# Optimization experiments

Hardware: AMD Instinct MI355X
Metric: run time of the kernel (lower is better)

## Reference

```python
import jax, jax.numpy as jnp
import numpy as np
from math import sqrt, pi

EMBED, HEADS, ATTN, MLP = 1024, 16, 1024, 4096
HEAD_DIM = ATTN // HEADS
EPS = 1e-5

def _ln(x):
    mu = jnp.mean(x, axis=-1, keepdims=True)
    var = jnp.var(x, axis=-1, keepdims=True)
    return (x - mu) / jnp.sqrt(var + EPS)

def _gelu(x):
    return 0.5 * x * (1.0 + jnp.tanh(sqrt(2.0 / pi) * (x + 0.044715 * x**3)))

def setup_inputs() -> dict:
    key = jax.random.key(0)
    ks = jax.random.split(key, 6)
    B, S = 2, 2048
    x = jax.random.normal(ks[0], (B, S, EMBED), dtype=jnp.float32)
    # weights stored as [in, out] (transpose of torch's [out, in]); math identical
    w_qkv = jax.random.normal(ks[1], (EMBED, 3 * ATTN), dtype=jnp.float32) / sqrt(EMBED)
    w_fc = jax.random.normal(ks[2], (ATTN, EMBED), dtype=jnp.float32) / sqrt(ATTN)
    w1 = jax.random.normal(ks[3], (EMBED, MLP), dtype=jnp.float32) / sqrt(EMBED)
    b1 = jnp.zeros((MLP,), dtype=jnp.float32)
    w2 = jax.random.normal(ks[4], (MLP, EMBED), dtype=jnp.float32) / sqrt(MLP)
    b2 = jnp.zeros((EMBED,), dtype=jnp.float32)
    return {"x": x, "w_qkv": w_qkv, "w_fc": w_fc, "w1": w1, "b1": b1, "w2": w2, "b2": b2}

def reference(x, w_qkv, w_fc, w1, b1, w2, b2):
    B, S, _ = x.shape
    res = x
    h = _ln(x)
    qkv = h @ w_qkv                                   # [B,S,3*ATTN]
    q, k, v = jnp.split(qkv, 3, axis=-1)
    q = q.reshape(B, S, HEADS, HEAD_DIM)
    k = k.reshape(B, S, HEADS, HEAD_DIM)
    v = v.reshape(B, S, HEADS, HEAD_DIM)
    attn = jnp.einsum('bqnc,bknc->bnqk', q, k) / sqrt(HEAD_DIM)  # [B,H,S,S]
    attn = jax.nn.softmax(attn, axis=-1)
    attn_val = jnp.einsum('bnqk,bknc->bqnc', attn, v).reshape(B, S, ATTN)
    x = res + attn_val @ w_fc
    res = x
    h = _ln(x)
    h = _gelu(h @ w1 + b1) @ w2 + b2
    return res + h
```

## Files before the change

### kernel.cpp

```cpp
#include <hip/hip_runtime.h>

typedef unsigned short u16;
typedef __attribute__((ext_vector_type(8))) short bf16x8;
typedef __attribute__((ext_vector_type(4))) short s16x4;
typedef __attribute__((ext_vector_type(4))) float f32x4;

#define DEV __device__ __forceinline__

DEV u16 f2bf(float f) {
  union { float f; unsigned u; } v; v.f = f;
  unsigned r = v.u + 0x7fffu + ((v.u >> 16) & 1u);
  return (u16)(r >> 16);
}
DEV u16 f2bf_tr(float f) {
  union { float f; unsigned u; } v; v.f = f;
  return (u16)(v.u >> 16);
}

DEV int swzi(int row, int col) { return row * 64 + (col ^ ((row & 7) << 3)); }

DEV void gl16(const u16* g, u16* l) {
  __builtin_amdgcn_global_load_lds((const __attribute__((address_space(1))) void*)g,
                                   (__attribute__((address_space(3))) void*)l, 16, 0, 0);
}

template <int N> DEV void waitv() {
  asm volatile("s_waitcnt vmcnt(%0)" :: "n"(N) : "memory");
}

__global__ __launch_bounds__(256) void wcastT(const float* __restrict__ w,
                                              u16* __restrict__ wt, int K, int N) {
  __shared__ float t[32][33];
  int n0 = blockIdx.x * 32, k0 = blockIdx.y * 32;
  int tx = threadIdx.x & 31, ty = threadIdx.x >> 5;
#pragma unroll
  for (int i = 0; i < 32; i += 8)
    t[ty + i][tx] = w[(size_t)(k0 + ty + i) * N + n0 + tx];
  __syncthreads();
#pragma unroll
  for (int i = 0; i < 32; i += 8)
    wt[(size_t)(n0 + ty + i) * K + k0 + tx] = f2bf(t[tx][ty + i]);
}

__global__ __launch_bounds__(256) void vtransp(const u16* __restrict__ v,
                                               u16* __restrict__ vt) {
  __shared__ u16 t[32][34];
  int s0 = blockIdx.x * 32, d0 = blockIdx.y * 32;
  int bh = blockIdx.z; int b = bh >> 4, h = bh & 15;
  int tx = threadIdx.x & 31, ty = threadIdx.x >> 5;
#pragma unroll
  for (int i = 0; i < 32; i += 8)
    t[ty + i][tx] = v[(size_t)(b * 2048 + s0 + ty + i) * 1024 + h * 64 + d0 + tx];
  __syncthreads();
#pragma unroll
  for (int i = 0; i < 32; i += 8)
    vt[((size_t)(b * 16 + h) * 64 + d0 + ty + i) * 2048 + s0 + tx] = t[tx][ty + i];
}

__global__ __launch_bounds__(256) void ln_kernel(const float* __restrict__ x,
                                                 u16* __restrict__ out) {
  int row = blockIdx.x, tid = threadIdx.x;
  const float4* xr = (const float4*)(x + (size_t)row * 1024);
  float4 f = xr[tid];
  float s = f.x + f.y + f.z + f.w;
  float s2 = f.x * f.x + f.y * f.y + f.z * f.z + f.w * f.w;
#pragma unroll
  for (int o = 1; o < 64; o <<= 1) { s += __shfl_xor(s, o); s2 += __shfl_xor(s2, o); }
  __shared__ float red[2][4];
  int wid = tid >> 6;
  if ((tid & 63) == 0) { red[0][wid] = s; red[1][wid] = s2; }
  __syncthreads();
  float tot  = red[0][0] + red[0][1] + red[0][2] + red[0][3];
  float tot2 = red[1][0] + red[1][1] + red[1][2] + red[1][3];
  float mu = tot * (1.0f / 1024.0f);
  float var = tot2 * (1.0f / 1024.0f) - mu * mu;
  float rstd = rsqrtf(var + 1e-5f);
  s16x4 o4;
  o4[0] = (short)f2bf((f.x - mu) * rstd);
  o4[1] = (short)f2bf((f.y - mu) * rstd);
  o4[2] = (short)f2bf((f.z - mu) * rstd);
  o4[3] = (short)f2bf((f.w - mu) * rstd);
  *(s16x4*)(out + (size_t)row * 1024 + tid * 4) = o4;
}

template <int MODE, int BM>
__global__ __launch_bounds__(256) void gemm_bt(
    const u16* __restrict__ A, const u16* __restrict__ Bt, int N, int K,
    const float* __restrict__ resid, const float* __restrict__ bias,
    float* __restrict__ outF, u16* __restrict__ o0, u16* __restrict__ o1,
    u16* __restrict__ o2) {
  constexpr int MR = BM / 32;
  constexpr int NBUF = (BM == 128) ? 3 : 4;
  constexpr int LDEPTH = BM / 64 + 2;
  constexpr int ASZ = BM * 32, BSZ = 128 * 32;
  __shared__ __align__(16) u16 lA[NBUF * ASZ];
  __shared__ __align__(16) u16 lB[NBUF * BSZ];
  int tid = threadIdx.x;
  int lane = tid & 63, wid = tid >> 6;
  int lr = lane & 15, lg = lane >> 4;

  int gx = gridDim.x;
  int nwg = gx * gridDim.y;
  int bid = blockIdx.y * gx + blockIdx.x;
  int swz = (bid & 7) * (nwg >> 3) + (bid >> 3);
  int rowBase = (swz / gx) * BM, colBase = (swz % gx) * 128;
  int wr = (wid >> 1) * (MR * 16), wc = (wid & 1) * 64;

  int srow = wid * 16 + (lane >> 2);
  int scol = (lane & 3) * 8;
  const u16* gA = A + (size_t)(rowBase + srow) * K + scol;
  const u16* gB = Bt + (size_t)(colBase + srow) * K + scol;
  u16* lAb = &lA[wid * 16 * 32];
  u16* lBb = &lB[wid * 16 * 32];

  auto stage = [&](int kk, int bidx) {
    u16* dA = lAb + bidx * ASZ;
    u16* dB = lBb + bidx * BSZ;
#pragma unroll
    for (int c = 0; c < BM / 64; c++)
      gl16(gA + (size_t)c * 64 * K + kk, dA + c * 64 * 32);
#pragma unroll
    for (int c = 0; c < 2; c++)
      gl16(gB + (size_t)c * 64 * K + kk, dB + c * 64 * 32);
  };

  f32x4 acc[MR][4];
  f32x4 zero = {0.f, 0.f, 0.f, 0.f};
#pragma unroll
  for (int m = 0; m < MR; m++)
#pragma unroll
    for (int n = 0; n < 4; n++) acc[m][n] = zero;

#pragma unroll
  for (int p = 0; p < NBUF - 1; p++) stage(p << 5, p);

  int nt = K >> 5;
  int cur = 0, stg = NBUF - 1;
  for (int t = 0; t < nt; t++) {
    int rem = nt - 1 - t;
    if (rem >= NBUF - 1) {
      stage((t + NBUF - 1) << 5, stg);
      waitv<(NBUF - 1) * LDEPTH>();
    } else if (rem == 2) {
      waitv<2 * LDEPTH>();
    } else if (rem == 1) {
      waitv<LDEPTH>();
    } else {
      waitv<0>();
    }
    __builtin_amdgcn_s_barrier();
    asm volatile("" ::: "memory");

    const u16* cA = &lA[cur * ASZ];
    const u16* cB = &lB[cur * BSZ];
    bf16x8 af[MR], bfv[4];
#pragma unroll
    for (int m = 0; m < MR; m++)
      af[m] = *(const bf16x8*)&cA[(wr + m * 16 + lr) * 32 + lg * 8];
#pragma unroll
    for (int n = 0; n < 4; n++)
      bfv[n] = *(const bf16x8*)&cB[(wc + n * 16 + lr) * 32 + lg * 8];
#pragma unroll
    for (int m = 0; m < MR; m++)
#pragma unroll
      for (int n = 0; n < 4; n++)
        acc[m][n] = __builtin_amdgcn_mfma_f32_16x16x32_bf16(bfv[n], af[m], acc[m][n], 0, 0, 0);

    asm volatile("" ::: "memory");
    __builtin_amdgcn_s_barrier();
    cur = (cur + 1 == NBUF) ? 0 : cur + 1;
    stg = (stg + 1 == NBUF) ? 0 : stg + 1;
  }

#pragma unroll
  for (int m = 0; m < MR; m++) {
    int grow = rowBase + wr + m * 16 + lr;
#pragma unroll
    for (int n = 0; n < 4; n++) {
      int gcol = colBase + wc + n * 16 + lg * 4;
      f32x4 v4 = acc[m][n];
      if constexpr (MODE == 0) {
        bool isq = gcol < 1024;
        u16* dst = isq ? o0 : ((gcol < 2048) ? o1 : o2);
        s16x4 o4;
#pragma unroll
        for (int j = 0; j < 4; j++)
          o4[j] = (short)f2bf(isq ? v4[j] * 0.18033688011112042f : v4[j]);
        *(s16x4*)&dst[(size_t)grow * 1024 + (gcol & 1023)] = o4;
      } else if constexpr (MODE == 1) {
        size_t idx = (size_t)grow * N + gcol;
        float4 r = *(const float4*)&resid[idx];
        float4 ov = {r.x + v4[0], r.y + v4[1], r.z + v4[2], r.w + v4[3]};
        *(float4*)&outF[idx] = ov;
      } else if constexpr (MODE == 2) {
        float4 bq = *(const float4*)&bias[gcol];
        s16x4 o4;
#pragma unroll
        for (int j = 0; j < 4; j++) {
          float g = v4[j] + ((const float*)&bq)[j];
          float e = __builtin_amdgcn_exp2f(2.302208198f * (g + 0.044715f * g * g * g));
          o4[j] = (short)f2bf(g - g * __builtin_amdgcn_rcpf(1.0f + e));
        }
        *(s16x4*)&o0[(size_t)grow * N + gcol] = o4;
      } else {
        size_t idx = (size_t)grow * N + gcol;
        float4 r = *(const float4*)&resid[idx];
        float4 bq = *(const float4*)&bias[gcol];
        float4 ov = {r.x + bq.x + v4[0], r.y + bq.y + v4[1],
                     r.z + bq.z + v4[2], r.w + bq.w + v4[3]};
        *(float4*)&outF[idx] = ov;
      }
    }
  }
}

__global__ __launch_bounds__(256) void attn_kernel(const u16* __restrict__ q,
                                                   const u16* __restrict__ k,
                                                   const u16* __restrict__ vt,
                                                   u16* __restrict__ o) {
  __shared__ __align__(16) u16 lK[64 * 64];
  __shared__ __align__(16) u16 lV[64 * 64];
  __shared__ __align__(16) u16 lP[4 * 2 * 16 * 64];
  const int S = 2048, E = 1024;
  int qt = blockIdx.x, h = blockIdx.y, b = blockIdx.z;
  int tid = threadIdx.x, wid = tid >> 6, lane = tid & 63;
  int lr = lane & 15, lg = lane >> 4;
  u16* lPw = &lP[wid * 2048];

  const u16* qp = q + ((size_t)b * S + qt * 128 + wid * 32) * E + h * 64;
  const u16* kp = k + (size_t)b * S * E + h * 64;
  const u16* vp = vt + ((size_t)(b * 16 + h) * 64) * S;

  bf16x8 aQ[2][2];
#pragma unroll
  for (int m = 0; m < 2; m++)
#pragma unroll
    for (int kk = 0; kk < 2; kk++)
      aQ[m][kk] = *(const bf16x8*)(qp + (size_t)(m * 16 + lr) * E + kk * 32 + lg * 8);

  bf16x8 onesv;
#pragma unroll
  for (int i = 0; i < 8; i++) onesv[i] = (short)0x3F80;

  f32x4 accO[2][4], accL[2];
  float Mx[2];
  f32x4 zero = {0.f, 0.f, 0.f, 0.f};
#pragma unroll
  for (int m = 0; m < 2; m++) {
    Mx[m] = -1e30f; accL[m] = zero;
#pragma unroll
    for (int nn = 0; nn < 4; nn++) accO[m][nn] = zero;
  }

  int sr_ = tid >> 3, sc_ = (tid & 7) * 8;
  const u16* kps0 = kp + (size_t)sr_ * E + sc_;
  const u16* kps1 = kp + (size_t)(sr_ + 32) * E + sc_;
  const u16* vps0 = vp + (size_t)sr_ * S + sc_;
  const u16* vps1 = vp + (size_t)(sr_ + 32) * S + sc_;

  bf16x8 rk0 = *(const bf16x8*)(kps0);
  bf16x8 rk1 = *(const bf16x8*)(kps1);
  bf16x8 rv0 = *(const bf16x8*)(vps0);
  bf16x8 rv1 = *(const bf16x8*)(vps1);

  for (int kv0 = 0; kv0 < S; kv0 += 64) {
    __syncthreads();
    *(bf16x8*)&lK[swzi(sr_, sc_)] = rk0;
    *(bf16x8*)&lK[swzi(32 + sr_, sc_)] = rk1;
    *(bf16x8*)&lV[swzi(sr_, sc_)] = rv0;
    *(bf16x8*)&lV[swzi(32 + sr_, sc_)] = rv1;
    int nx = kv0 + 64;
    if (nx < S) {
      rk0 = *(const bf16x8*)(kps0 + (size_t)nx * E);
      rk1 = *(const bf16x8*)(kps1 + (size_t)nx * E);
      rv0 = *(const bf16x8*)(vps0 + nx);
      rv1 = *(const bf16x8*)(vps1 + nx);
    }
    __syncthreads();

    f32x4 sc4[2][4];
#pragma unroll
    for (int m = 0; m < 2; m++)
#pragma unroll
      for (int n = 0; n < 4; n++) sc4[m][n] = zero;
#pragma unroll
    for (int n = 0; n < 4; n++) {
      bf16x8 bk0 = *(const bf16x8*)&lK[swzi(n * 16 + lr, lg * 8)];
      bf16x8 bk1 = *(const bf16x8*)&lK[swzi(n * 16 + lr, 32 + lg * 8)];
#pragma unroll
      for (int m = 0; m < 2; m++) {
        sc4[m][n] = __builtin_amdgcn_mfma_f32_16x16x32_bf16(bk0, aQ[m][0], sc4[m][n], 0, 0, 0);
        sc4[m][n] = __builtin_amdgcn_mfma_f32_16x16x32_bf16(bk1, aQ[m][1], sc4[m][n], 0, 0, 0);
      }
    }

    float mxr[2];
#pragma unroll
    for (int m = 0; m < 2; m++) {
      float a0 = fmaxf(fmaxf(sc4[m][0][0], sc4[m][0][1]), fmaxf(sc4[m][0][2], sc4[m][0][3]));
      float a1 = fmaxf(fmaxf(sc4[m][1][0], sc4[m][1][1]), fmaxf(sc4[m][1][2], sc4[m][1][3]));
      float a2 = fmaxf(fmaxf(sc4[m][2][0], sc4[m][2][1]), fmaxf(sc4[m][2][2], sc4[m][2][3]));
      float a3 = fmaxf(fmaxf(sc4[m][3][0], sc4[m][3][1]), fmaxf(sc4[m][3][2], sc4[m][3][3]));
      float mx = fmaxf(fmaxf(a0, a1), fmaxf(a2, a3));
      mx = fmaxf(mx, __shfl_xor(mx, 16));
      mx = fmaxf(mx, __shfl_xor(mx, 32));
      mxr[m] = mx;
    }
    bool need = (mxr[0] > Mx[0] + 8.f) || (mxr[1] > Mx[1] + 8.f);
    if (__any(need)) {
#pragma unroll
      for (int m = 0; m < 2; m++) {
        float nm = fmaxf(Mx[m], mxr[m]);
        float s = __builtin_amdgcn_exp2f(Mx[m] - nm);
        Mx[m] = nm;
        accL[m] *= s;
#pragma unroll
        for (int nn = 0; nn < 4; nn++) accO[m][nn] *= s;
      }
    }
#pragma unroll
    for (int m = 0; m < 2; m++)
#pragma unroll
      for (int n = 0; n < 4; n++) {
        s16x4 pq;
#pragma unroll
        for (int j = 0; j < 4; j++)
          pq[j] = (short)f2bf_tr(__builtin_amdgcn_exp2f(sc4[m][n][j] - Mx[m]));
        *(s16x4*)&lPw[m * 1024 + swzi(lr, n * 16 + lg * 4)] = pq;
      }

#pragma unroll
    for (int kk = 0; kk < 2; kk++) {
      bf16x8 ap[2];
#pragma unroll
      for (int m = 0; m < 2; m++)
        ap[m] = *(const bf16x8*)&lPw[m * 1024 + swzi(lr, kk * 32 + lg * 8)];
#pragma unroll
      for (int m = 0; m < 2; m++)
        accL[m] = __builtin_amdgcn_mfma_f32_16x16x32_bf16(onesv, ap[m], accL[m], 0, 0, 0);
#pragma unroll
      for (int nn = 0; nn < 4; nn++) {
        bf16x8 bv = *(const bf16x8*)&lV[swzi(nn * 16 + lr, kk * 32 + lg * 8)];
#pragma unroll
        for (int m = 0; m < 2; m++)
          accO[m][nn] = __builtin_amdgcn_mfma_f32_16x16x32_bf16(bv, ap[m], accO[m][nn], 0, 0, 0);
      }
    }
  }

#pragma unroll
  for (int m = 0; m < 2; m++) {
    float inv = __builtin_amdgcn_rcpf(accL[m][0]);
    int srow = qt * 128 + wid * 32 + m * 16 + lr;
#pragma unroll
    for (int nn = 0; nn < 4; nn++) {
      s16x4 o4;
#pragma unroll
      for (int j = 0; j < 4; j++) o4[j] = (short)f2bf(accO[m][nn][j] * inv);
      *(s16x4*)&o[((size_t)b * S + srow) * E + h * 64 + nn * 16 + lg * 4] = o4;
    }
  }
}

extern "C" void kernel_launch(void* const* d_in, const int* in_sizes, int n_in,
                              void* d_out, int out_size, void* d_ws, size_t ws_size,
                              hipStream_t stream) {
  (void)in_sizes; (void)n_in; (void)out_size; (void)ws_size;
  const float* x     = (const float*)d_in[0];
  const float* w_qkv = (const float*)d_in[1];
  const float* w_fc  = (const float*)d_in[2];
  const float* w1    = (const float*)d_in[3];
  const float* b1    = (const float*)d_in[4];
  const float* w2    = (const float*)d_in[5];
  const float* b2    = (const float*)d_in[6];
  float* out = (float*)d_out;
  char* ws = (char*)d_ws;

  u16* wqkvT = (u16*)(ws);
  u16* wfcT  = (u16*)(ws + 6291456);
  u16* w1T   = (u16*)(ws + 8388608);
  u16* w2T   = (u16*)(ws + 16777216);
  u16* hbuf  = (u16*)(ws + 25165824);
  u16* qbuf  = (u16*)(ws + 33554432);
  u16* kbuf  = (u16*)(ws + 41943040);
  u16* vbuf  = (u16*)(ws + 50331648);
  u16* vtbuf = (u16*)(ws + 58720256);
  float* x2  = (float*)(ws + 67108864);
  u16* act   = qbuf;

  wcastT<<<dim3(96, 32), 256, 0, stream>>>(w_qkv, wqkvT, 1024, 3072);
  wcastT<<<dim3(32, 32), 256, 0, stream>>>(w_fc, wfcT, 1024, 1024);
  wcastT<<<dim3(128, 32), 256, 0, stream>>>(w1, w1T, 1024, 4096);
  wcastT<<<dim3(32, 128), 256, 0, stream>>>(w2, w2T, 4096, 1024);

  ln_kernel<<<4096, 256, 0, stream>>>(x, hbuf);
  gemm_bt<0, 128><<<dim3(24, 32), 256, 0, stream>>>(hbuf, wqkvT, 3072, 1024,
                                                    nullptr, nullptr, nullptr, qbuf, kbuf, vbuf);
  vtransp<<<dim3(64, 2, 32), 256, 0, stream>>>(vbuf, vtbuf);
  attn_kernel<<<dim3(16, 16, 2), 256, 0, stream>>>(qbuf, kbuf, vtbuf, hbuf);
  gemm_bt<1, 64><<<dim3(8, 64), 256, 0, stream>>>(hbuf, wfcT, 1024, 1024,
                                                  x, nullptr, x2, nullptr, nullptr, nullptr);
  ln_kernel<<<4096, 256, 0, stream>>>(x2, hbuf);
  gemm_bt<2, 128><<<dim3(32, 32), 256, 0, stream>>>(hbuf, w1T, 4096, 1024,
                                                    nullptr, b1, nullptr, act, nullptr, nullptr);
  gemm_bt<3, 64><<<dim3(8, 64), 256, 0, stream>>>(act, w2T, 1024, 4096,
                                                  x2, b2, out, nullptr, nullptr, nullptr);
}
```

Baseline: 271.6 us.

## Add 256x256-tile 512-thread GEMM for QKV and FC1 projections

```diff
diff --git a/kernel.cpp b/kernel.cpp
--- a/kernel.cpp
+++ b/kernel.cpp
@@ -83,12 +83,117 @@
   *(s16x4*)(out + (size_t)row * 1024 + tid * 4) = o4;
 }
 
+template <int MODE>
+__global__ __launch_bounds__(512) void gemm256(
+    const u16* __restrict__ A, const u16* __restrict__ Bt, int N, int K,
+    const float* __restrict__ bias,
+    u16* __restrict__ o0, u16* __restrict__ o1, u16* __restrict__ o2) {
+  __shared__ __align__(16) u16 lA[4 * 256 * 32];
+  __shared__ __align__(16) u16 lB[4 * 256 * 32];
+  int tid = threadIdx.x;
+  int lane = tid & 63, wid = tid >> 6;
+  int lr = lane & 15, lg = lane >> 4;
+  int wm = wid >> 2, wn = wid & 3;
+
+  int gx = gridDim.x;
+  int nwg = gx * gridDim.y;
+  int bid = blockIdx.y * gx + blockIdx.x;
+  int swz = (bid & 7) * (nwg >> 3) + (bid >> 3);
+  int rowBase = (swz / gx) * 256, colBase = (swz % gx) * 256;
+
+  int srow = wid * 32 + (lane >> 2);
+  int scol = (lane & 3) * 8;
+  const u16* gA = A + (size_t)(rowBase + srow) * K + scol;
+  const u16* gB = Bt + (size_t)(colBase + srow) * K + scol;
+  u16* lAw = lA + wid * 32 * 32;
+  u16* lBw = lB + wid * 32 * 32;
+
+  auto stageHalf = [&](int h) {
+    int slot = ((h >> 1) & 1) * 2 + (h & 1);
+    int koff = (h >> 1) * 64 + (h & 1) * 32;
+    u16* dA = lAw + slot * 8192;
+    u16* dB = lBw + slot * 8192;
+    gl16(gA + koff, dA);
+    gl16(gA + (size_t)16 * K + koff, dA + 16 * 32);
+    gl16(gB + koff, dB);
+    gl16(gB + (size_t)16 * K + koff, dB + 16 * 32);
+  };
+
+  f32x4 acc[8][4];
+  f32x4 zero = {0.f, 0.f, 0.f, 0.f};
+#pragma unroll
+  for (int m = 0; m < 8; m++)
+#pragma unroll
+    for (int n = 0; n < 4; n++) acc[m][n] = zero;
+
+  stageHalf(0); stageHalf(1); stageHalf(2);
+
+  int NH = (K >> 6) * 2;
+  for (int h = 0; h < NH; h++) {
+    int rem = NH - 1 - h;
+    if (rem >= 3) { stageHalf(h + 3); waitv<12>(); }
+    else if (rem == 2) { waitv<8>(); }
+    else if (rem == 1) { waitv<4>(); }
+    else { waitv<0>(); }
+    __builtin_amdgcn_s_barrier();
+    asm volatile("" ::: "memory");
+
+    int slot = ((h >> 1) & 1) * 2 + (h & 1);
+    const u16* pA = lA + slot * 8192;
+    const u16* pB = lB + slot * 8192;
+    bf16x8 bfv[4], af[8];
+#pragma unroll
+    for (int n = 0; n < 4; n++)
+      bfv[n] = *(const bf16x8*)&pB[(wn * 64 + n * 16 + lr) * 32 + lg * 8];
+#pragma unroll
+    for (int m = 0; m < 8; m++)
+      af[m] = *(const bf16x8*)&pA[(wm * 128 + m * 16 + lr) * 32 + lg * 8];
+    __builtin_amdgcn_s_setprio(1);
+#pragma unroll
+    for (int m = 0; m < 8; m++)
+#pragma unroll
+      for (int n = 0; n < 4; n++)
+        acc[m][n] = __builtin_amdgcn_mfma_f32_16x16x32_bf16(bfv[n], af[m], acc[m][n], 0, 0, 0);
+    __builtin_amdgcn_s_setprio(0);
+    asm volatile("" ::: "memory");
+    __builtin_amdgcn_s_barrier();
+  }
+
+#pragma unroll
+  for (int m = 0; m < 8; m++) {
+    int grow = rowBase + wm * 128 + m * 16 + lr;
+#pragma unroll
+    for (int n = 0; n < 4; n++) {
+      int gcol = colBase + wn * 64 + n * 16 + lg * 4;
+      f32x4 v4 = acc[m][n];
+      if constexpr (MODE == 0) {
+        bool isq = gcol < 1024;
+        u16* dst = isq ? o0 : ((gcol < 2048) ? o1 : o2);
+        s16x4 o4;
+#pragma unroll
+        for (int j = 0; j < 4; j++)
+          o4[j] = (short)f2bf(isq ? v4[j] * 0.18033688011112042f : v4[j]);
+        *(s16x4*)&dst[(size_t)grow * 1024 + (gcol & 1023)] = o4;
+      } else {
+        float4 bq = *(const float4*)&bias[gcol];
+        s16x4 o4;
+#pragma unroll
+        for (int j = 0; j < 4; j++) {
+          float g = v4[j] + ((const float*)&bq)[j];
+          float e = __builtin_amdgcn_exp2f(2.302208198f * (g + 0.044715f * g * g * g));
+          o4[j] = (short)f2bf(g - g * __builtin_amdgcn_rcpf(1.0f + e));
+        }
+        *(s16x4*)&o0[(size_t)grow * N + gcol] = o4;
+      }
+    }
+  }
+}
+
 template <int MODE, int BM>
 __global__ __launch_bounds__(256) void gemm_bt(
     const u16* __restrict__ A, const u16* __restrict__ Bt, int N, int K,
     const float* __restrict__ resid, const float* __restrict__ bias,
-    float* __restrict__ outF, u16* __restrict__ o0, u16* __restrict__ o1,
-    u16* __restrict__ o2) {
+    float* __restrict__ outF) {
   constexpr int MR = BM / 32;
   constexpr int NBUF = (BM == 128) ? 3 : 4;
   constexpr int LDEPTH = BM / 64 + 2;
@@ -179,29 +284,11 @@
     for (int n = 0; n < 4; n++) {
       int gcol = colBase + wc + n * 16 + lg * 4;
       f32x4 v4 = acc[m][n];
-      if constexpr (MODE == 0) {
-        bool isq = gcol < 1024;
-        u16* dst = isq ? o0 : ((gcol < 2048) ? o1 : o2);
-        s16x4 o4;
-#pragma unroll
-        for (int j = 0; j < 4; j++)
-          o4[j] = (short)f2bf(isq ? v4[j] * 0.18033688011112042f : v4[j]);
-        *(s16x4*)&dst[(size_t)grow * 1024 + (gcol & 1023)] = o4;
-      } else if constexpr (MODE == 1) {
+      if constexpr (MODE == 1) {
         size_t idx = (size_t)grow * N + gcol;
         float4 r = *(const float4*)&resid[idx];
         float4 ov = {r.x + v4[0], r.y + v4[1], r.z + v4[2], r.w + v4[3]};
         *(float4*)&outF[idx] = ov;
-      } else if constexpr (MODE == 2) {
-        float4 bq = *(const float4*)&bias[gcol];
-        s16x4 o4;
-#pragma unroll
-        for (int j = 0; j < 4; j++) {
-          float g = v4[j] + ((const float*)&bq)[j];
-          float e = __builtin_amdgcn_exp2f(2.302208198f * (g + 0.044715f * g * g * g));
-          o4[j] = (short)f2bf(g - g * __builtin_amdgcn_rcpf(1.0f + e));
-        }
-        *(s16x4*)&o0[(size_t)grow * N + gcol] = o4;
       } else {
         size_t idx = (size_t)grow * N + gcol;
         float4 r = *(const float4*)&resid[idx];
@@ -394,15 +481,15 @@
   wcastT<<<dim3(32, 128), 256, 0, stream>>>(w2, w2T, 4096, 1024);
 
   ln_kernel<<<4096, 256, 0, stream>>>(x, hbuf);
-  gemm_bt<0, 128><<<dim3(24, 32), 256, 0, stream>>>(hbuf, wqkvT, 3072, 1024,
-                                                    nullptr, nullptr, nullptr, qbuf, kbuf, vbuf);
+  gemm256<0><<<dim3(12, 16), 512, 0, stream>>>(hbuf, wqkvT, 3072, 1024,
+                                               nullptr, qbuf, kbuf, vbuf);
   vtransp<<<dim3(64, 2, 32), 256, 0, stream>>>(vbuf, vtbuf);
   attn_kernel<<<dim3(16, 16, 2), 256, 0, stream>>>(qbuf, kbuf, vtbuf, hbuf);
   gemm_bt<1, 64><<<dim3(8, 64), 256, 0, stream>>>(hbuf, wfcT, 1024, 1024,
-                                                  x, nullptr, x2, nullptr, nullptr, nullptr);
+                                                  x, nullptr, x2);
   ln_kernel<<<4096, 256, 0, stream>>>(x2, hbuf);
-  gemm_bt<2, 128><<<dim3(32, 32), 256, 0, stream>>>(hbuf, w1T, 4096, 1024,
-                                                    nullptr, b1, nullptr, act, nullptr, nullptr);
+  gemm256<2><<<dim3(16, 16), 512, 0, stream>>>(hbuf, w1T, 4096, 1024,
+                                               b1, act, nullptr, nullptr);
   gemm_bt<3, 64><<<dim3(8, 64), 256, 0, stream>>>(act, w2T, 1024, 4096,
-                                                  x2, b2, out, nullptr, nullptr, nullptr);
-}
+                                                  x2, b2, out);
+}
```

After: 286.8 us. 5.6% more time.
